# Optimization experiments

Measured on AMD Instinct MI355X. Metric: run time of the kernel, lower is better.

The kernel has to match this reference:

```python
import jax, jax.numpy as jnp
import numpy as np

N, E, F_IN, HID, HEADS, OUT = 50000, 800000, 128, 64, 4, 40


def gat_layer(x, src, dst, n, W, a_src, a_dst, b, heads, ch):
    # PyG GATConv: h = x @ W per head; e_ij = LeakyReLU(a_src.h_j + a_dst.h_i)
    h = (x @ W).reshape(n, heads, ch)
    al_s = jnp.einsum('nhc,hc->nh', h, a_src)  # source-side logit term
    al_d = jnp.einsum('nhc,hc->nh', h, a_dst)  # target-side logit term
    e = jax.nn.leaky_relu(al_s[src] + al_d[dst], negative_slope=0.2)  # [E,H]
    m = jax.ops.segment_max(e, dst, num_segments=n)  # stable softmax per target node
    e = jnp.exp(e - m[dst])
    s = jax.ops.segment_sum(e, dst, num_segments=n)
    alpha = e / s[dst]  # [E,H]
    out = jax.ops.segment_sum(h[src] * alpha[:, :, None], dst, num_segments=n)  # [n,H,C]
    return out.reshape(n, heads * ch) + b


def gat_forward(x, src, dst, W0, as0, ad0, b0, W1, as1, ad1, b1, W2, as2, ad2, b2):
    n = x.shape[0]
    x = jax.nn.elu(gat_layer(x, src, dst, n, W0, as0, ad0, b0, HEADS, HID))
    x = jax.nn.elu(gat_layer(x, src, dst, n, W1, as1, ad1, b1, HEADS, HID))
    x = gat_layer(x, src, dst, n, W2, as2, ad2, b2, 1, OUT)
    return jax.nn.log_softmax(x, axis=1)


def setup_inputs() -> dict:
    key = jax.random.key(0)
    ks = jax.random.split(key, 16)
    x = jax.random.normal(ks[0], (N, F_IN), dtype=jnp.float32)
    edge_index = jax.random.randint(ks[1], (2, E), 0, N, dtype=jnp.int64)
    g = lambda k, sh: jax.random.normal(k, sh, dtype=jnp.float32) * (1.0 / np.sqrt(sh[0]))
    d_hid = HID * HEADS
    return {
        'x': x, 'edge_index': edge_index,
        'W0': g(ks[2], (F_IN, d_hid)), 'as0': g(ks[3], (HEADS, HID)), 'ad0': g(ks[4], (HEADS, HID)), 'b0': jnp.zeros((d_hid,), jnp.float32),
        'W1': g(ks[5], (d_hid, d_hid)), 'as1': g(ks[6], (HEADS, HID)), 'ad1': g(ks[7], (HEADS, HID)), 'b1': jnp.zeros((d_hid,), jnp.float32),
        'W2': g(ks[8], (d_hid, OUT)), 'as2': g(ks[9], (1, OUT)), 'ad2': g(ks[10], (1, OUT)), 'b2': jnp.zeros((OUT,), jnp.float32),
    }


def reference(x, edge_index, W0, as0, ad0, b0, W1, as1, ad1, b1, W2, as2, ad2, b2):
    n = x.shape[0]
    loops = jnp.arange(n, dtype=edge_index.dtype)  # PyG add_self_loops=True
    src = jnp.concatenate([edge_index[0], loops])
    dst = jnp.concatenate([edge_index[1], loops])
    return gat_forward(x, src, dst, W0, as0, ad0, b0, W1, as1, ad1, b1, W2, as2, ad2, b2)
```

## Files before the change

### kernel.cpp

```cpp
#include <hip/hip_runtime.h>
#include <hip/hip_fp16.h>
#include <math.h>

#define NODES 50000
#define NEDGES 800000
#define TOT_E (NEDGES + NODES)
#define SCAN_B 256
#define SCAN_NB ((NODES + SCAN_B - 1) / SCAN_B)

typedef __attribute__((ext_vector_type(8))) _Float16 half8v;
typedef __attribute__((ext_vector_type(4))) float f32x4;

union U2H { uint u; __half2 h; };

static __device__ __forceinline__ float lrelu(float z) {
  return z > 0.f ? z : 0.2f * z;
}
static __device__ __forceinline__ ushort f2h(float f) {
  __half h = __float2half_rn(f);
  return *reinterpret_cast<ushort*>(&h);
}
static __device__ __forceinline__ void wave_lds_fence() {
  __builtin_amdgcn_wave_barrier();
  asm volatile("s_waitcnt lgkmcnt(0)" ::: "memory");
  __builtin_amdgcn_sched_barrier(0);
}

__global__ void k_hist(const int* __restrict__ dst, int* __restrict__ counts) {
  int stride = gridDim.x * blockDim.x;
  for (int i = blockIdx.x * blockDim.x + threadIdx.x; i < TOT_E; i += stride) {
    int d = (i < NEDGES) ? dst[i] : (i - NEDGES);
    atomicAdd(&counts[d], 1);
  }
}

__global__ __launch_bounds__(SCAN_B) void k_scan_red(const int* __restrict__ counts,
                                                     int* __restrict__ bsum) {
  __shared__ int sm[SCAN_B];
  int idx = blockIdx.x * SCAN_B + threadIdx.x;
  int v = (idx < NODES) ? counts[idx] : 0;
  sm[threadIdx.x] = v;
  __syncthreads();
  for (int off = SCAN_B / 2; off > 0; off >>= 1) {
    if (threadIdx.x < off) sm[threadIdx.x] += sm[threadIdx.x + off];
    __syncthreads();
  }
  if (threadIdx.x == 0) bsum[blockIdx.x] = sm[0];
}

__global__ __launch_bounds__(256) void k_scan_part(const int* __restrict__ bsum,
                                                   int* __restrict__ bpre) {
  __shared__ int sm[256];
  int tid = threadIdx.x;
  int v = (tid < SCAN_NB) ? bsum[tid] : 0;
  sm[tid] = v;
  __syncthreads();
  for (int off = 1; off < 256; off <<= 1) {
    int t = (tid >= off) ? sm[tid - off] : 0;
    __syncthreads();
    sm[tid] += t;
    __syncthreads();
  }
  if (tid < SCAN_NB) bpre[tid] = sm[tid] - v;
}

__global__ __launch_bounds__(SCAN_B) void k_scan_emit(const int* __restrict__ counts,
    const int* __restrict__ bpre, int* __restrict__ offs, int* __restrict__ cur) {
  __shared__ int sm[SCAN_B];
  int idx = blockIdx.x * SCAN_B + threadIdx.x;
  int tid = threadIdx.x;
  int v = (idx < NODES) ? counts[idx] : 0;
  sm[tid] = v;
  __syncthreads();
  for (int off = 1; off < SCAN_B; off <<= 1) {
    int t = (tid >= off) ? sm[tid - off] : 0;
    __syncthreads();
    sm[tid] += t;
    __syncthreads();
  }
  int base = bpre[blockIdx.x];
  int excl = base + sm[tid] - v;
  if (idx < NODES) { offs[idx] = excl; cur[idx] = excl; }
  if (idx == NODES - 1) offs[NODES] = excl + v;
}

__global__ void k_scatter(const int* __restrict__ src, const int* __restrict__ dst,
                          int* __restrict__ cur, int* __restrict__ ssrc) {
  int stride = gridDim.x * blockDim.x;
  for (int i = blockIdx.x * blockDim.x + threadIdx.x; i < TOT_E; i += stride) {
    int s, d;
    if (i < NEDGES) { s = src[i]; d = dst[i]; } else { s = i - NEDGES; d = s; }
    int pos = atomicAdd(&cur[d], 1);
    ssrc[pos] = s;
  }
}

__global__ void k_cast4(const float* __restrict__ X, ushort* __restrict__ Xh, int total4) {
  int stride = gridDim.x * blockDim.x;
  for (int i = blockIdx.x * blockDim.x + threadIdx.x; i < total4; i += stride) {
    float4 v = *(const float4*)&X[i * 4];
    ushort4 o;
    o.x = f2h(v.x); o.y = f2h(v.y); o.z = f2h(v.z); o.w = f2h(v.w);
    *(ushort4*)&Xh[i * 4] = o;
  }
}

__global__ void k_packB(const float* __restrict__ W, ushort* __restrict__ Bp,
                        int N, int NF, int total) {
  int idx = blockIdx.x * blockDim.x + threadIdx.x;
  if (idx >= total) return;
  int i = idx & 7;
  int lane = (idx >> 3) & 63;
  int rem = idx >> 9;
  int nf = rem % NF;
  int kf = rem / NF;
  int k = kf * 32 + (lane >> 4) * 8 + i;
  int col = nf * 16 + (lane & 15);
  float v = (col < N) ? W[(size_t)k * N + col] : 0.f;
  Bp[idx] = f2h(v);
}

template<int KF, int NFW, int CG, int HEADS, int NF_TOT>
__global__ __launch_bounds__(256, 2) void k_gemm_reg(
    const ushort* __restrict__ A, const ushort* __restrict__ Bp,
    ushort* __restrict__ H, const float* __restrict__ a_s, const float* __restrict__ a_d,
    float* __restrict__ al_s, float* __restrict__ al_d, int M, int N, int K) {
  int wave = (blockIdx.x * blockDim.x + threadIdx.x) >> 6;
  int lane = threadIdx.x & 63;
  int lg = lane >> 4;
  int lr = lane & 15;
  int total_waves = (gridDim.x * blockDim.x) >> 6;
  int wpc = total_waves / CG;
  int cg = wave / wpc;
  int mslot = wave - cg * wpc;
  if (cg >= CG) return;

  half8v b[KF][NFW];
#pragma unroll
  for (int kf = 0; kf < KF; ++kf)
#pragma unroll
    for (int n = 0; n < NFW; ++n)
      b[kf][n] = *(const half8v*)(Bp + ((size_t)(kf * NF_TOT + cg * NFW + n) * 64 + lane) * 8);

  float asc[NFW], adc[NFW];
#pragma unroll
  for (int n = 0; n < NFW; ++n) {
    int col = (cg * NFW + n) * 16 + lr;
    bool ok = col < N;
    asc[n] = ok ? a_s[col] : 0.f;
    adc[n] = ok ? a_d[col] : 0.f;
  }

  int nstrips = M >> 4;
  for (int strip = mslot; strip < nstrips; strip += wpc) {
    const ushort* arow = A + (size_t)(strip * 16 + lr) * K + lg * 8;
    half8v a[KF];
#pragma unroll
    for (int kf = 0; kf < KF; ++kf) a[kf] = *(const half8v*)(arow + kf * 32);
    f32x4 acc[NFW];
#pragma unroll
    for (int n = 0; n < NFW; ++n) acc[n] = (f32x4){0.f, 0.f, 0.f, 0.f};
#pragma unroll
    for (int kf = 0; kf < KF; ++kf)
#pragma unroll
      for (int n = 0; n < NFW; ++n)
        acc[n] = __builtin_amdgcn_mfma_f32_16x16x32_f16(a[kf], b[kf][n], acc[n], 0, 0, 0);

#pragma unroll
    for (int n = 0; n < NFW; ++n) {
      int col = (cg * NFW + n) * 16 + lr;
      if (col < N) {
#pragma unroll
        for (int r = 0; r < 4; ++r) {
          int row = strip * 16 + lg * 4 + r;
          H[(size_t)row * N + col] = f2h(acc[n][r]);
        }
      }
    }

    float ps[4], pd[4];
#pragma unroll
    for (int r = 0; r < 4; ++r) {
      float s = 0.f, d = 0.f;
#pragma unroll
      for (int n = 0; n < NFW; ++n) {
        s += acc[n][r] * asc[n];
        d += acc[n][r] * adc[n];
      }
      ps[r] = s; pd[r] = d;
    }
#pragma unroll
    for (int off = 1; off <= 8; off <<= 1)
#pragma unroll
      for (int t = 0; t < 4; ++t) {
        ps[t] += __shfl_xor(ps[t], off);
        pd[t] += __shfl_xor(pd[t], off);
      }
    if (lr < 4) {
      int row = strip * 16 + lg * 4 + lr;
      if (HEADS == 4) {
        al_s[row * 4 + cg] = ps[lr];
        al_d[row * 4 + cg] = pd[lr];
      } else {
        al_s[row] = ps[lr];
        al_d[row] = pd[lr];
      }
    }
  }
}

__global__ __launch_bounds__(256) void k_agg4(const ushort* __restrict__ hb,
    const float* __restrict__ al_s, const float* __restrict__ al_d,
    const int* __restrict__ offs, const int* __restrict__ ssrc,
    const float* __restrict__ bias, ushort* __restrict__ outb) {
  __shared__ int s_idx[4][64];
  __shared__ uint s_alp[4][256];
  int w = threadIdx.x >> 6;
  int wid = (blockIdx.x * blockDim.x + threadIdx.x) >> 6;
  if (wid >= NODES) return;
  int lane = threadIdx.x & 63;
  int beg = offs[wid], end = offs[wid + 1];
  float4 ald4 = *(const float4*)&al_d[wid * 4];

  float m[4], s[4];
#pragma unroll
  for (int h = 0; h < 4; ++h) { m[h] = -1e30f; s[h] = 0.f; }
  for (int i = beg + lane; i < end; i += 64) {
    int sv = ssrc[i];
    float4 a4 = *(const float4*)&al_s[sv * 4];
    float z[4] = {lrelu(a4.x + ald4.x), lrelu(a4.y + ald4.y),
                  lrelu(a4.z + ald4.z), lrelu(a4.w + ald4.w)};
#pragma unroll
    for (int h = 0; h < 4; ++h) {
      if (z[h] > m[h]) { s[h] = s[h] * __expf(m[h] - z[h]) + 1.f; m[h] = z[h]; }
      else s[h] += __expf(z[h] - m[h]);
    }
  }
#pragma unroll
  for (int off = 1; off <= 32; off <<= 1) {
#pragma unroll
    for (int h = 0; h < 4; ++h) {
      float mo = __shfl_xor(m[h], off), so = __shfl_xor(s[h], off);
      float mn = fmaxf(m[h], mo);
      s[h] = s[h] * __expf(m[h] - mn) + so * __expf(mo - mn);
      m[h] = mn;
    }
  }
  float inv[4];
#pragma unroll
  for (int h = 0; h < 4; ++h) inv[h] = 1.f / s[h];

  int half = lane >> 5;
  int cl = lane & 31;
  int hh = cl >> 3;
  __half2 z2 = __float2half2_rn(0.f);
  __half2 acc2a[4] = {z2, z2, z2, z2};
  __half2 acc2b[4] = {z2, z2, z2, z2};

  for (int cb = beg; cb < end; cb += 64) {
    int cnt = min(64, end - cb);
    wave_lds_fence();
    if (lane < cnt) {
      int sv = ssrc[cb + lane];
      float4 a4 = *(const float4*)&al_s[sv * 4];
      U2H p0, p1, p2, p3;
      p0.h = __float2half2_rn(__expf(lrelu(a4.x + ald4.x) - m[0]) * inv[0]);
      p1.h = __float2half2_rn(__expf(lrelu(a4.y + ald4.y) - m[1]) * inv[1]);
      p2.h = __float2half2_rn(__expf(lrelu(a4.z + ald4.z) - m[2]) * inv[2]);
      p3.h = __float2half2_rn(__expf(lrelu(a4.w + ald4.w) - m[3]) * inv[3]);
      s_idx[w][lane] = sv;
      uint4 pk = make_uint4(p0.u, p1.u, p2.u, p3.u);
      *(uint4*)&s_alp[w][lane * 4] = pk;
    }
    wave_lds_fence();
    int e = half;
    for (; e + 2 < cnt; e += 4) {
      int sv0 = s_idx[w][e], sv1 = s_idx[w][e + 2];
      U2H a0, a1;
      a0.u = s_alp[w][e * 4 + hh];
      a1.u = s_alp[w][(e + 2) * 4 + hh];
      uint4 hv0 = *(const uint4*)(hb + (size_t)sv0 * 256 + cl * 8);
      uint4 hv1 = *(const uint4*)(hb + (size_t)sv1 * 256 + cl * 8);
      U2H v;
      v.u = hv0.x; acc2a[0] = __hfma2(a0.h, v.h, acc2a[0]);
      v.u = hv0.y; acc2a[1] = __hfma2(a0.h, v.h, acc2a[1]);
      v.u = hv0.z; acc2a[2] = __hfma2(a0.h, v.h, acc2a[2]);
      v.u = hv0.w; acc2a[3] = __hfma2(a0.h, v.h, acc2a[3]);
      v.u = hv1.x; acc2b[0] = __hfma2(a1.h, v.h, acc2b[0]);
      v.u = hv1.y; acc2b[1] = __hfma2(a1.h, v.h, acc2b[1]);
      v.u = hv1.z; acc2b[2] = __hfma2(a1.h, v.h, acc2b[2]);
      v.u = hv1.w; acc2b[3] = __hfma2(a1.h, v.h, acc2b[3]);
    }
    for (; e < cnt; e += 2) {
      int sv = s_idx[w][e];
      U2H a0; a0.u = s_alp[w][e * 4 + hh];
      uint4 hv = *(const uint4*)(hb + (size_t)sv * 256 + cl * 8);
      U2H v;
      v.u = hv.x; acc2a[0] = __hfma2(a0.h, v.h, acc2a[0]);
      v.u = hv.y; acc2a[1] = __hfma2(a0.h, v.h, acc2a[1]);
      v.u = hv.z; acc2a[2] = __hfma2(a0.h, v.h, acc2a[2]);
      v.u = hv.w; acc2a[3] = __hfma2(a0.h, v.h, acc2a[3]);
    }
  }
  ushort4 ores[2];
#pragma unroll
  for (int j = 0; j < 4; ++j) {
    U2H t; t.h = __hadd2(acc2a[j], acc2b[j]);
    U2H o; o.u = __shfl_xor(t.u, 32);
    t.h = __hadd2(t.h, o.h);
    float lo = __low2float(t.h) + bias[cl * 16 / 2 + j * 2];
    float hi = __high2float(t.h) + bias[cl * 8 + j * 2 + 1];
    lo = lo > 0.f ? lo : __expf(lo) - 1.f;
    hi = hi > 0.f ? hi : __expf(hi) - 1.f;
    ((ushort*)ores)[j * 2]     = f2h(lo);
    ((ushort*)ores)[j * 2 + 1] = f2h(hi);
  }
  if (half == 0) {
    *(ushort4*)(outb + (size_t)wid * 256 + cl * 8)     = ores[0];
    *(ushort4*)(outb + (size_t)wid * 256 + cl * 8 + 4) = ores[1];
  }
}

__global__ __launch_bounds__(256) void k_agg1(const ushort* __restrict__ hb,
    const float* __restrict__ al_s, const float* __restrict__ al_d,
    const int* __restrict__ offs, const int* __restrict__ ssrc,
    const float* __restrict__ bias, float* __restrict__ out) {
  __shared__ int s_idx[4][64];
  __shared__ uint s_alp[4][64];
  int w = threadIdx.x >> 6;
  int wid = (blockIdx.x * blockDim.x + threadIdx.x) >> 6;
  if (wid >= NODES) return;
  int lane = threadIdx.x & 63;
  int beg = offs[wid], end = offs[wid + 1];
  float ald = al_d[wid];

  float m = -1e30f, s = 0.f;
  for (int i = beg + lane; i < end; i += 64) {
    float z = lrelu(al_s[ssrc[i]] + ald);
    if (z > m) { s = s * __expf(m - z) + 1.f; m = z; }
    else s += __expf(z - m);
  }
#pragma unroll
  for (int off = 1; off <= 32; off <<= 1) {
    float mo = __shfl_xor(m, off), so = __shfl_xor(s, off);
    float mn = fmaxf(m, mo);
    s = s * __expf(m - mn) + so * __expf(mo - mn);
    m = mn;
  }
  float inv = 1.f / s;

  int q = lane >> 4;
  int cq = lane & 15;
  bool act = cq < 10;
  __half2 z2 = __float2half2_rn(0.f);
  __half2 acc2a[2] = {z2, z2};
  __half2 acc2b[2] = {z2, z2};
  for (int cb = beg; cb < end; cb += 64) {
    int cnt = min(64, end - cb);
    wave_lds_fence();
    if (lane < cnt) {
      int sv = ssrc[cb + lane];
      U2H p; p.h = __float2half2_rn(__expf(lrelu(al_s[sv] + ald) - m) * inv);
      s_idx[w][lane] = sv;
      s_alp[w][lane] = p.u;
    }
    wave_lds_fence();
    int e = q;
    for (; e + 4 < cnt; e += 8) {
      int sv0 = s_idx[w][e], sv1 = s_idx[w][e + 4];
      U2H a0, a1;
      a0.u = s_alp[w][e];
      a1.u = s_alp[w][e + 4];
      if (act) {
        uint2 hv0 = *(const uint2*)(hb + (size_t)sv0 * 40 + cq * 4);
        uint2 hv1 = *(const uint2*)(hb + (size_t)sv1 * 40 + cq * 4);
        U2H v;
        v.u = hv0.x; acc2a[0] = __hfma2(a0.h, v.h, acc2a[0]);
        v.u = hv0.y; acc2a[1] = __hfma2(a0.h, v.h, acc2a[1]);
        v.u = hv1.x; acc2b[0] = __hfma2(a1.h, v.h, acc2b[0]);
        v.u = hv1.y; acc2b[1] = __hfma2(a1.h, v.h, acc2b[1]);
      }
    }
    for (; e < cnt; e += 4) {
      int sv = s_idx[w][e];
      U2H a0; a0.u = s_alp[w][e];
      if (act) {
        uint2 hv = *(const uint2*)(hb + (size_t)sv * 40 + cq * 4);
        U2H v;
        v.u = hv.x; acc2a[0] = __hfma2(a0.h, v.h, acc2a[0]);
        v.u = hv.y; acc2a[1] = __hfma2(a0.h, v.h, acc2a[1]);
      }
    }
  }
  float vv[4];
#pragma unroll
  for (int j = 0; j < 2; ++j) {
    U2H t; t.h = __hadd2(acc2a[j], acc2b[j]);
    U2H o;
    o.u = __shfl_xor(t.u, 16); t.h = __hadd2(t.h, o.h);
    o.u = __shfl_xor(t.u, 32); t.h = __hadd2(t.h, o.h);
    vv[j * 2]     = __low2float(t.h);
    vv[j * 2 + 1] = __high2float(t.h);
  }
  float mm = -1e30f;
  if (act) {
#pragma unroll
    for (int j = 0; j < 4; ++j) {
      vv[j] += bias[cq * 4 + j];
      mm = fmaxf(mm, vv[j]);
    }
  }
#pragma unroll
  for (int off = 1; off <= 8; off <<= 1) mm = fmaxf(mm, __shfl_xor(mm, off));
  float se = 0.f;
  if (act) {
#pragma unroll
    for (int j = 0; j < 4; ++j) se += __expf(vv[j] - mm);
  }
#pragma unroll
  for (int off = 1; off <= 8; off <<= 1) se += __shfl_xor(se, off);
  if (act && q == 0) {
    float lse = mm + __logf(se);
    float4 o;
    o.x = vv[0] - lse; o.y = vv[1] - lse; o.z = vv[2] - lse; o.w = vv[3] - lse;
    *(float4*)&out[(size_t)wid * 40 + cq * 4] = o;
  }
}

extern "C" void kernel_launch(void* const* d_in, const int* in_sizes, int n_in,
                              void* d_out, int out_size, void* d_ws, size_t ws_size,
                              hipStream_t stream) {
  const float* x   = (const float*)d_in[0];
  const int*   ei  = (const int*)d_in[1];
  const float* W0  = (const float*)d_in[2];
  const float* as0 = (const float*)d_in[3];
  const float* ad0 = (const float*)d_in[4];
  const float* b0  = (const float*)d_in[5];
  const float* W1  = (const float*)d_in[6];
  const float* as1 = (const float*)d_in[7];
  const float* ad1 = (const float*)d_in[8];
  const float* b1  = (const float*)d_in[9];
  const float* W2  = (const float*)d_in[10];
  const float* as2 = (const float*)d_in[11];
  const float* ad2 = (const float*)d_in[12];
  const float* b2  = (const float*)d_in[13];
  float* out = (float*)d_out;

  char* p = (char*)d_ws;
  auto take = [&](size_t bytes) {
    char* q = p;
    p += (bytes + 255) & ~(size_t)255;
    return (void*)q;
  };
  ushort* xb0 = (ushort*)take((size_t)NODES * 128 * 2);
  ushort* xb1 = (ushort*)take((size_t)NODES * 256 * 2);
  ushort* xb2 = (ushort*)take((size_t)NODES * 256 * 2);
  ushort* hb  = (ushort*)take((size_t)NODES * 256 * 2);
  float* als  = (float*)take((size_t)NODES * 4 * 4);
  float* ald  = (float*)take((size_t)NODES * 4 * 4);
  int* ssrc   = (int*)take((size_t)TOT_E * 4);
  int* offs   = (int*)take((size_t)(NODES + 1) * 4);
  int* cur    = (int*)take((size_t)NODES * 4);
  int* cnt    = (int*)take((size_t)NODES * 4);
  int* bsum   = (int*)take((size_t)SCAN_NB * 4);
  int* bpre   = (int*)take((size_t)SCAN_NB * 4);
  ushort* Bp0 = (ushort*)take((size_t)4 * 16 * 512 * 2);
  ushort* Bp1 = (ushort*)take((size_t)8 * 16 * 512 * 2);
  ushort* Bp2 = (ushort*)take((size_t)8 * 3 * 512 * 2);

  hipMemsetAsync(cnt, 0, (size_t)NODES * 4, stream);
  k_hist<<<2048, 256, 0, stream>>>(ei + NEDGES, cnt);
  k_scan_red<<<SCAN_NB, SCAN_B, 0, stream>>>(cnt, bsum);
  k_scan_part<<<1, 256, 0, stream>>>(bsum, bpre);
  k_scan_emit<<<SCAN_NB, SCAN_B, 0, stream>>>(cnt, bpre, offs, cur);
  k_scatter<<<2048, 256, 0, stream>>>(ei, ei + NEDGES, cur, ssrc);

  k_cast4<<<2048, 256, 0, stream>>>(x, xb0, NODES * 128 / 4);
  {
    int t0 = 4 * 16 * 512;  k_packB<<<(t0 + 255) / 256, 256, 0, stream>>>(W0, Bp0, 256, 16, t0);
    int t1 = 8 * 16 * 512;  k_packB<<<(t1 + 255) / 256, 256, 0, stream>>>(W1, Bp1, 256, 16, t1);
    int t2 = 8 * 3 * 512;   k_packB<<<(t2 + 255) / 256, 256, 0, stream>>>(W2, Bp2, 40, 3, t2);
  }

  int nwb = (NODES * 64 + 255) / 256;
  int ggb = 512;

  k_gemm_reg<4, 4, 4, 4, 16><<<ggb, 256, 0, stream>>>(xb0, Bp0, hb, as0, ad0, als, ald, NODES, 256, 128);
  k_agg4<<<nwb, 256, 0, stream>>>(hb, als, ald, offs, ssrc, b0, xb1);

  k_gemm_reg<8, 4, 4, 4, 16><<<ggb, 256, 0, stream>>>(xb1, Bp1, hb, as1, ad1, als, ald, NODES, 256, 256);
  k_agg4<<<nwb, 256, 0, stream>>>(hb, als, ald, offs, ssrc, b1, xb2);

  k_gemm_reg<8, 3, 1, 1, 3><<<ggb, 256, 0, stream>>>(xb2, Bp2, hb, as2, ad2, als, ald, NODES, 40, 256);
  k_agg1<<<nwb, 256, 0, stream>>>(hb, als, ald, offs, ssrc, b2, out);
}
```

Measured before the change: 328.7 us.

## Defer softmax normalization and pack edge index with weights in LDS

```diff
diff --git a/kernel.cpp b/kernel.cpp
--- a/kernel.cpp
+++ b/kernel.cpp
@@ -125,15 +125,13 @@
     const ushort* __restrict__ A, const ushort* __restrict__ Bp,
     ushort* __restrict__ H, const float* __restrict__ a_s, const float* __restrict__ a_d,
     float* __restrict__ al_s, float* __restrict__ al_d, int M, int N, int K) {
-  int wave = (blockIdx.x * blockDim.x + threadIdx.x) >> 6;
+  int wib = threadIdx.x >> 6;
   int lane = threadIdx.x & 63;
   int lg = lane >> 4;
   int lr = lane & 15;
-  int total_waves = (gridDim.x * blockDim.x) >> 6;
-  int wpc = total_waves / CG;
-  int cg = wave / wpc;
-  int mslot = wave - cg * wpc;
-  if (cg >= CG) return;
+  int cg, strip0, sstride;
+  if (CG == 4) { cg = wib; strip0 = blockIdx.x; sstride = gridDim.x; }
+  else { cg = 0; strip0 = blockIdx.x * 4 + wib; sstride = gridDim.x * 4; }
 
   half8v b[KF][NFW];
 #pragma unroll
@@ -152,7 +150,7 @@
   }
 
   int nstrips = M >> 4;
-  for (int strip = mslot; strip < nstrips; strip += wpc) {
+  for (int strip = strip0; strip < nstrips; strip += sstride) {
     const ushort* arow = A + (size_t)(strip * 16 + lr) * K + lg * 8;
     half8v a[KF];
 #pragma unroll
@@ -213,8 +211,7 @@
     const float* __restrict__ al_s, const float* __restrict__ al_d,
     const int* __restrict__ offs, const int* __restrict__ ssrc,
     const float* __restrict__ bias, ushort* __restrict__ outb) {
-  __shared__ int s_idx[4][64];
-  __shared__ uint s_alp[4][256];
+  __shared__ uint4 s_pack[4][64][2];
   int w = threadIdx.x >> 6;
   int wid = (blockIdx.x * blockDim.x + threadIdx.x) >> 6;
   if (wid >= NODES) return;
@@ -222,37 +219,26 @@
   int beg = offs[wid], end = offs[wid + 1];
   float4 ald4 = *(const float4*)&al_d[wid * 4];
 
-  float m[4], s[4];
-#pragma unroll
-  for (int h = 0; h < 4; ++h) { m[h] = -1e30f; s[h] = 0.f; }
+  float m[4] = {-1e30f, -1e30f, -1e30f, -1e30f};
   for (int i = beg + lane; i < end; i += 64) {
     int sv = ssrc[i];
     float4 a4 = *(const float4*)&al_s[sv * 4];
-    float z[4] = {lrelu(a4.x + ald4.x), lrelu(a4.y + ald4.y),
-                  lrelu(a4.z + ald4.z), lrelu(a4.w + ald4.w)};
-#pragma unroll
-    for (int h = 0; h < 4; ++h) {
-      if (z[h] > m[h]) { s[h] = s[h] * __expf(m[h] - z[h]) + 1.f; m[h] = z[h]; }
-      else s[h] += __expf(z[h] - m[h]);
-    }
+    m[0] = fmaxf(m[0], lrelu(a4.x + ald4.x));
+    m[1] = fmaxf(m[1], lrelu(a4.y + ald4.y));
+    m[2] = fmaxf(m[2], lrelu(a4.z + ald4.z));
+    m[3] = fmaxf(m[3], lrelu(a4.w + ald4.w));
   }
 #pragma unroll
   for (int off = 1; off <= 32; off <<= 1) {
 #pragma unroll
-    for (int h = 0; h < 4; ++h) {
-      float mo = __shfl_xor(m[h], off), so = __shfl_xor(s[h], off);
-      float mn = fmaxf(m[h], mo);
-      s[h] = s[h] * __expf(m[h] - mn) + so * __expf(mo - mn);
-      m[h] = mn;
-    }
-  }
-  float inv[4];
-#pragma unroll
-  for (int h = 0; h < 4; ++h) inv[h] = 1.f / s[h];
+    for (int h = 0; h < 4; ++h) m[h] = fmaxf(m[h], __shfl_xor(m[h], off));
+  }
 
   int half = lane >> 5;
   int cl = lane & 31;
   int hh = cl >> 3;
+  uint clb = (uint)cl * 8;
+  float sacc[4] = {0.f, 0.f, 0.f, 0.f};
   __half2 z2 = __float2half2_rn(0.f);
   __half2 acc2a[4] = {z2, z2, z2, z2};
   __half2 acc2b[4] = {z2, z2, z2, z2};
@@ -261,26 +247,28 @@
     int cnt = min(64, end - cb);
     wave_lds_fence();
     if (lane < cnt) {
-      int sv = ssrc[cb + lane];
+      uint sv = (uint)ssrc[cb + lane];
       float4 a4 = *(const float4*)&al_s[sv * 4];
+      float t0 = __expf(lrelu(a4.x + ald4.x) - m[0]);
+      float t1 = __expf(lrelu(a4.y + ald4.y) - m[1]);
+      float t2 = __expf(lrelu(a4.z + ald4.z) - m[2]);
+      float t3 = __expf(lrelu(a4.w + ald4.w) - m[3]);
+      sacc[0] += t0; sacc[1] += t1; sacc[2] += t2; sacc[3] += t3;
       U2H p0, p1, p2, p3;
-      p0.h = __float2half2_rn(__expf(lrelu(a4.x + ald4.x) - m[0]) * inv[0]);
-      p1.h = __float2half2_rn(__expf(lrelu(a4.y + ald4.y) - m[1]) * inv[1]);
-      p2.h = __float2half2_rn(__expf(lrelu(a4.z + ald4.z) - m[2]) * inv[2]);
-      p3.h = __float2half2_rn(__expf(lrelu(a4.w + ald4.w) - m[3]) * inv[3]);
-      s_idx[w][lane] = sv;
-      uint4 pk = make_uint4(p0.u, p1.u, p2.u, p3.u);
-      *(uint4*)&s_alp[w][lane * 4] = pk;
+      p0.h = __float2half2_rn(t0); p1.h = __float2half2_rn(t1);
+      p2.h = __float2half2_rn(t2); p3.h = __float2half2_rn(t3);
+      s_pack[w][lane][0] = make_uint4(sv, p0.u, sv, p1.u);
+      s_pack[w][lane][1] = make_uint4(sv, p2.u, sv, p3.u);
     }
     wave_lds_fence();
     int e = half;
     for (; e + 2 < cnt; e += 4) {
-      int sv0 = s_idx[w][e], sv1 = s_idx[w][e + 2];
-      U2H a0, a1;
-      a0.u = s_alp[w][e * 4 + hh];
-      a1.u = s_alp[w][(e + 2) * 4 + hh];
-      uint4 hv0 = *(const uint4*)(hb + (size_t)sv0 * 256 + cl * 8);
-      uint4 hv1 = *(const uint4*)(hb + (size_t)sv1 * 256 + cl * 8);
+      const uint2* pk0 = (const uint2*)&s_pack[w][e][0];
+      const uint2* pk1 = (const uint2*)&s_pack[w][e + 2][0];
+      uint2 k0 = pk0[hh], k1 = pk1[hh];
+      U2H a0, a1; a0.u = k0.y; a1.u = k1.y;
+      uint4 hv0 = *(const uint4*)(hb + ((k0.x << 8) + clb));
+      uint4 hv1 = *(const uint4*)(hb + ((k1.x << 8) + clb));
       U2H v;
       v.u = hv0.x; acc2a[0] = __hfma2(a0.h, v.h, acc2a[0]);
       v.u = hv0.y; acc2a[1] = __hfma2(a0.h, v.h, acc2a[1]);
@@ -292,9 +280,10 @@
       v.u = hv1.w; acc2b[3] = __hfma2(a1.h, v.h, acc2b[3]);
     }
     for (; e < cnt; e += 2) {
-      int sv = s_idx[w][e];
-      U2H a0; a0.u = s_alp[w][e * 4 + hh];
-      uint4 hv = *(const uint4*)(hb + (size_t)sv * 256 + cl * 8);
+      const uint2* pk = (const uint2*)&s_pack[w][e][0];
+      uint2 k0 = pk[hh];
+      U2H a0; a0.u = k0.y;
+      uint4 hv = *(const uint4*)(hb + ((k0.x << 8) + clb));
       U2H v;
       v.u = hv.x; acc2a[0] = __hfma2(a0.h, v.h, acc2a[0]);
       v.u = hv.y; acc2a[1] = __hfma2(a0.h, v.h, acc2a[1]);
@@ -302,14 +291,20 @@
       v.u = hv.w; acc2a[3] = __hfma2(a0.h, v.h, acc2a[3]);
     }
   }
+#pragma unroll
+  for (int off = 1; off <= 32; off <<= 1) {
+#pragma unroll
+    for (int h = 0; h < 4; ++h) sacc[h] += __shfl_xor(sacc[h], off);
+  }
+  float invs = 1.f / sacc[hh];
   ushort4 ores[2];
 #pragma unroll
   for (int j = 0; j < 4; ++j) {
     U2H t; t.h = __hadd2(acc2a[j], acc2b[j]);
     U2H o; o.u = __shfl_xor(t.u, 32);
     t.h = __hadd2(t.h, o.h);
-    float lo = __low2float(t.h) + bias[cl * 16 / 2 + j * 2];
-    float hi = __high2float(t.h) + bias[cl * 8 + j * 2 + 1];
+    float lo = __low2float(t.h) * invs + bias[cl * 8 + j * 2];
+    float hi = __high2float(t.h) * invs + bias[cl * 8 + j * 2 + 1];
     lo = lo > 0.f ? lo : __expf(lo) - 1.f;
     hi = hi > 0.f ? hi : __expf(hi) - 1.f;
     ((ushort*)ores)[j * 2]     = f2h(lo);
@@ -325,8 +320,7 @@
     const float* __restrict__ al_s, const float* __restrict__ al_d,
     const int* __restrict__ offs, const int* __restrict__ ssrc,
     const float* __restrict__ bias, float* __restrict__ out) {
-  __shared__ int s_idx[4][64];
-  __shared__ uint s_alp[4][64];
+  __shared__ uint2 s_pack[4][64];
   int w = threadIdx.x >> 6;
   int wid = (blockIdx.x * blockDim.x + threadIdx.x) >> 6;
   if (wid >= NODES) return;
@@ -334,24 +328,17 @@
   int beg = offs[wid], end = offs[wid + 1];
   float ald = al_d[wid];
 
-  float m = -1e30f, s = 0.f;
-  for (int i = beg + lane; i < end; i += 64) {
-    float z = lrelu(al_s[ssrc[i]] + ald);
-    if (z > m) { s = s * __expf(m - z) + 1.f; m = z; }
-    else s += __expf(z - m);
-  }
-#pragma unroll
-  for (int off = 1; off <= 32; off <<= 1) {
-    float mo = __shfl_xor(m, off), so = __shfl_xor(s, off);
-    float mn = fmaxf(m, mo);
-    s = s * __expf(m - mn) + so * __expf(mo - mn);
-    m = mn;
-  }
-  float inv = 1.f / s;
+  float m = -1e30f;
+  for (int i = beg + lane; i < end; i += 64)
+    m = fmaxf(m, lrelu(al_s[ssrc[i]] + ald));
+#pragma unroll
+  for (int off = 1; off <= 32; off <<= 1) m = fmaxf(m, __shfl_xor(m, off));
 
   int q = lane >> 4;
   int cq = lane & 15;
   bool act = cq < 10;
+  uint cqb = (uint)cq * 4;
+  float sacc = 0.f;
   __half2 z2 = __float2half2_rn(0.f);
   __half2 acc2a[2] = {z2, z2};
   __half2 acc2b[2] = {z2, z2};
@@ -359,21 +346,20 @@
     int cnt = min(64, end - cb);
     wave_lds_fence();
     if (lane < cnt) {
-      int sv = ssrc[cb + lane];
-      U2H p; p.h = __float2half2_rn(__expf(lrelu(al_s[sv] + ald) - m) * inv);
-      s_idx[w][lane] = sv;
-      s_alp[w][lane] = p.u;
+      uint sv = (uint)ssrc[cb + lane];
+      float t = __expf(lrelu(al_s[sv] + ald) - m);
+      sacc += t;
+      U2H p; p.h = __float2half2_rn(t);
+      s_pack[w][lane] = make_uint2(sv, p.u);
     }
     wave_lds_fence();
     int e = q;
     for (; e + 4 < cnt; e += 8) {
-      int sv0 = s_idx[w][e], sv1 = s_idx[w][e + 4];
-      U2H a0, a1;
-      a0.u = s_alp[w][e];
-      a1.u = s_alp[w][e + 4];
+      uint2 k0 = s_pack[w][e], k1 = s_pack[w][e + 4];
+      U2H a0, a1; a0.u = k0.y; a1.u = k1.y;
       if (act) {
-        uint2 hv0 = *(const uint2*)(hb + (size_t)sv0 * 40 + cq * 4);
-        uint2 hv1 = *(const uint2*)(hb + (size_t)sv1 * 40 + cq * 4);
+        uint2 hv0 = *(const uint2*)(hb + (k0.x * 40u + cqb));
+        uint2 hv1 = *(const uint2*)(hb + (k1.x * 40u + cqb));
         U2H v;
         v.u = hv0.x; acc2a[0] = __hfma2(a0.h, v.h, acc2a[0]);
         v.u = hv0.y; acc2a[1] = __hfma2(a0.h, v.h, acc2a[1]);
@@ -382,16 +368,19 @@
       }
     }
     for (; e < cnt; e += 4) {
-      int sv = s_idx[w][e];
-      U2H a0; a0.u = s_alp[w][e];
+      uint2 k0 = s_pack[w][e];
+      U2H a0; a0.u = k0.y;
       if (act) {
-        uint2 hv = *(const uint2*)(hb + (size_t)sv * 40 + cq * 4);
+        uint2 hv = *(const uint2*)(hb + (k0.x * 40u + cqb));
         U2H v;
         v.u = hv.x; acc2a[0] = __hfma2(a0.h, v.h, acc2a[0]);
         v.u = hv.y; acc2a[1] = __hfma2(a0.h, v.h, acc2a[1]);
       }
     }
   }
+#pragma unroll
+  for (int off = 1; off <= 32; off <<= 1) sacc += __shfl_xor(sacc, off);
+  float invs = 1.f / sacc;
   float vv[4];
 #pragma unroll
   for (int j = 0; j < 2; ++j) {
@@ -399,8 +388,8 @@
     U2H o;
     o.u = __shfl_xor(t.u, 16); t.h = __hadd2(t.h, o.h);
     o.u = __shfl_xor(t.u, 32); t.h = __hadd2(t.h, o.h);
-    vv[j * 2]     = __low2float(t.h);
-    vv[j * 2 + 1] = __high2float(t.h);
+    vv[j * 2]     = __low2float(t.h) * invs;
+    vv[j * 2 + 1] = __high2float(t.h) * invs;
   }
   float mm = -1e30f;
   if (act) {
@@ -483,14 +472,13 @@
   }
 
   int nwb = (NODES * 64 + 255) / 256;
-  int ggb = 512;
-
-  k_gemm_reg<4, 4, 4, 4, 16><<<ggb, 256, 0, stream>>>(xb0, Bp0, hb, as0, ad0, als, ald, NODES, 256, 128);
+
+  k_gemm_reg<4, 4, 4, 4, 16><<<512, 256, 0, stream>>>(xb0, Bp0, hb, as0, ad0, als, ald, NODES, 256, 128);
   k_agg4<<<nwb, 256, 0, stream>>>(hb, als, ald, offs, ssrc, b0, xb1);
 
-  k_gemm_reg<8, 4, 4, 4, 16><<<ggb, 256, 0, stream>>>(xb1, Bp1, hb, as1, ad1, als, ald, NODES, 256, 256);
+  k_gemm_reg<8, 4, 4, 4, 16><<<512, 256, 0, stream>>>(xb1, Bp1, hb, as1, ad1, als, ald, NODES, 256, 256);
   k_agg4<<<nwb, 256, 0, stream>>>(hb, als, ald, offs, ssrc, b1, xb2);
 
-  k_gemm_reg<8, 3, 1, 1, 3><<<ggb, 256, 0, stream>>>(xb2, Bp2, hb, as2, ad2, als, ald, NODES, 40, 256);
+  k_gemm_reg<8, 3, 1, 1, 3><<<512, 256, 0, stream>>>(xb2, Bp2, hb, as2, ad2, als, ald, NODES, 40, 256);
   k_agg1<<<nwb, 256, 0, stream>>>(hb, als, ald, offs, ssrc, b2, out);
 }
```

Result: no change. 334.5 us (+1.8%).
